# Kernel tuning notes

Hardware: AMD Instinct MI355X
Metric: run time of the kernel (lower is better)

Reference implementation:

```python
import jax, jax.numpy as jnp
import numpy as np

H = 16          # num heads
HD = 88         # head dim = 1408 / 16
IMG = 336
PATCH = 14
THETA = 10000.0
IDX = IMG // PATCH          # 24 patches per side
SEQ = IDX * IDX + 1         # 576 patches + 1 CLS slot = 577


def _vision_rope_cos_sin():
    # Faithful to HF Llama4VisionRotaryEmbedding (rope_type='llama4', complex64):
    # 2D rope over (x, y) patch coordinates; CLS token gets zero rotation.
    img_idx = np.arange(IDX * IDX, dtype=np.int64).reshape(-1, 1)
    img_idx = np.concatenate([img_idx, img_idx[:1]], axis=0)
    img_idx[-1, -1] = -2  # CLS token marker
    fx = img_idx % IDX
    fy = img_idx // IDX
    freq_dim = HD // 2  # 44
    rope_freq = 1.0 / (THETA ** (np.arange(0, freq_dim, 2)[: freq_dim // 2].astype(np.float64) / freq_dim))
    freqs_x = np.repeat((fx + 1)[..., None] * rope_freq[None, None, :], 2, axis=-1)
    freqs_y = np.repeat((fy + 1)[..., None] * rope_freq[None, None, :], 2, axis=-1)
    freqs = np.concatenate([freqs_x, freqs_y], axis=-1)[..., ::2]  # [SEQ, 1, HD//2]
    freqs = np.where(img_idx.reshape(-1, 1, 1) < 0, 0.0, freqs)
    return jnp.asarray(np.cos(freqs), jnp.float32), jnp.asarray(np.sin(freqs), jnp.float32)


def _apply_rope(x, cos, sin):
    # x: [B, S, H, HD]; treat last dim as HD//2 complex pairs, rotate by e^{i*freq}
    xr = x.reshape(*x.shape[:-1], HD // 2, 2)
    a, b = xr[..., 0], xr[..., 1]               # [B, S, H, HD//2]
    out_r = a * cos - b * sin                   # cos/sin [S,1,HD//2] broadcast over B,H
    out_i = a * sin + b * cos
    return jnp.stack([out_r, out_i], axis=-1).reshape(x.shape)


def setup_inputs() -> dict:
    key = jax.random.key(0)
    ks = jax.random.split(key, 9)
    D = H * HD  # 1408
    B, S = 32, SEQ
    s = 0.02
    return {
        "hidden_states": jax.random.normal(ks[0], (B, S, D), jnp.float32),
        "wq": jax.random.normal(ks[1], (D, D), jnp.float32) * s,
        "bq": jax.random.normal(ks[2], (D,), jnp.float32) * s,
        "wk": jax.random.normal(ks[3], (D, D), jnp.float32) * s,
        "bk": jax.random.normal(ks[4], (D,), jnp.float32) * s,
        "wv": jax.random.normal(ks[5], (D, D), jnp.float32) * s,
        "bv": jax.random.normal(ks[6], (D,), jnp.float32) * s,
        "wo": jax.random.normal(ks[7], (D, D), jnp.float32) * s,
        "bo": jax.random.normal(ks[8], (D,), jnp.float32) * s,
    }


def reference(hidden_states, wq, bq, wk, bk, wv, bv, wo, bo):
    B, S, D = hidden_states.shape
    cos, sin = _vision_rope_cos_sin()
    # QKV projections (torch Linear convention: y = x @ W.T + b)
    q = (hidden_states @ wq.T + bq).reshape(B, S, H, HD)
    k = (hidden_states @ wk.T + bk).reshape(B, S, H, HD)
    v = (hidden_states @ wv.T + bv).reshape(B, S, H, HD)
    q = _apply_rope(q, cos, sin)
    k = _apply_rope(k, cos, sin)
    # Full (non-causal) self-attention
    scores = jnp.einsum('bqhd,bkhd->bhqk', q, k) * (HD ** -0.5)
    probs = jax.nn.softmax(scores, axis=-1)
    attn = jnp.einsum('bhqk,bkhd->bqhd', probs, v).reshape(B, S, D)
    return attn @ wo.T + bo
```

## Files before the change

kernel.cpp:

```cpp
#include <hip/hip_runtime.h>
#include <hip/hip_bf16.h>
#include <cstdint>
#include <cstddef>

#define NHEADS 16
#define HDIM   88
#define SEQLEN 577
#define NBATCH 32
#define DMODEL 1408
#define MROWS  (NBATCH * SEQLEN)
#define MTILES 145
#define MPAD   (MTILES * 128)
#define SP     592
#define DP     96
#define NFREQ  44
#define NBH    (NBATCH * NHEADS)

typedef __attribute__((ext_vector_type(8))) short short8;
typedef __attribute__((ext_vector_type(4))) float floatx4;

__device__ __forceinline__ unsigned short f2bf(float f) {
    union { float f; unsigned u; } v; v.f = f;
    unsigned u = v.u;
    u += 0x7fffu + ((u >> 16) & 1u);
    return (unsigned short)(u >> 16);
}

__device__ __forceinline__ void gload_lds16(const void* g, void* lds) {
    __builtin_amdgcn_global_load_lds(
        (__attribute__((address_space(1))) unsigned int*)(void*)(g ? (void*)g : (void*)g),
        (__attribute__((address_space(3))) unsigned int*)lds, 16, 0, 0);
}

__global__ void l4v_rope_table(float* __restrict__ cos_t, float* __restrict__ sin_t) {
    int idx = blockIdx.x * blockDim.x + threadIdx.x;
    if (idx >= SEQLEN * NFREQ) return;
    int s = idx / NFREQ, j = idx % NFREQ;
    float ang = 0.0f;
    if (s != SEQLEN - 1) {
        int coord = (j < 22) ? (s % 24) : (s / 24);
        int i = (j < 22) ? j : j - 22;
        float rf = __expf(-(2.0f * (float)i / 44.0f) * 9.21034037197618f);
        ang = (float)(coord + 1) * rf;
    }
    cos_t[idx] = cosf(ang);
    sin_t[idx] = sinf(ang);
}

__global__ void l4v_cvt_bf16(const float* __restrict__ in, unsigned short* __restrict__ out, int n) {
    int i = (blockIdx.x * blockDim.x + threadIdx.x) * 4;
    if (i + 3 < n) {
        float4 f = *(const float4*)(in + i);
        ushort4 o;
        o.x = f2bf(f.x); o.y = f2bf(f.y); o.z = f2bf(f.z); o.w = f2bf(f.w);
        *(ushort4*)(out + i) = o;
    } else {
        for (; i < n; i++) out[i] = f2bf(in[i]);
    }
}

__global__ __launch_bounds__(256, 2)
void l4v_gemm128(const unsigned short* __restrict__ A,
                 const unsigned short* __restrict__ Bw,
                 const float* __restrict__ bias,
                 const float* __restrict__ cos_t,
                 const float* __restrict__ sin_t,
                 unsigned short* __restrict__ out_bf,
                 float* __restrict__ out_f32,
                 int mode)
{
    __shared__ __align__(16) unsigned short a_sm[128 * 32];
    __shared__ __align__(16) unsigned short b_sm[128 * 32];

    const int tid  = threadIdx.x;
    const int lane = tid & 63;
    const int w    = tid >> 6;
    const int quad = lane >> 4;
    const int c    = lane & 15;
    const int wr   = w >> 1;
    const int wc   = w & 1;
    const int m0   = blockIdx.y * 128;
    const int n0   = blockIdx.x * 128;

    floatx4 acc[4][4];
#pragma unroll
    for (int i = 0; i < 4; i++)
#pragma unroll
        for (int j = 0; j < 4; j++) acc[i][j] = (floatx4)0.0f;

    const int chunk0 = w * 128 + lane;
    const int chunk1 = w * 128 + 64 + lane;
    const int r0 = chunk0 >> 2, ch0 = chunk0 & 3;
    const int r1 = chunk1 >> 2, ch1 = chunk1 & 3;
    const unsigned short* Ab = A  + (size_t)m0 * DMODEL;
    const unsigned short* Bb = Bw + (size_t)n0 * DMODEL;

    for (int k0 = 0; k0 < DMODEL; k0 += 32) {
        gload_lds16(Ab + (size_t)r0 * DMODEL + k0 + ch0 * 8, a_sm + (w * 128) * 8);
        gload_lds16(Ab + (size_t)r1 * DMODEL + k0 + ch1 * 8, a_sm + (w * 128 + 64) * 8);
        gload_lds16(Bb + (size_t)r0 * DMODEL + k0 + ch0 * 8, b_sm + (w * 128) * 8);
        gload_lds16(Bb + (size_t)r1 * DMODEL + k0 + ch1 * 8, b_sm + (w * 128 + 64) * 8);
        __syncthreads();
        short8 af[4], bfr[4];
#pragma unroll
        for (int mt = 0; mt < 4; mt++)
            af[mt] = *(const short8*)(a_sm + (wr * 64 + mt * 16 + c) * 32 + quad * 8);
#pragma unroll
        for (int nt = 0; nt < 4; nt++)
            bfr[nt] = *(const short8*)(b_sm + (wc * 64 + nt * 16 + c) * 32 + quad * 8);
#pragma unroll
        for (int mt = 0; mt < 4; mt++)
#pragma unroll
            for (int nt = 0; nt < 4; nt++)
                acc[mt][nt] = __builtin_amdgcn_mfma_f32_16x16x32_bf16(af[mt], bfr[nt], acc[mt][nt], 0, 0, 0);
        __syncthreads();
    }

    if (mode == 3) {
#pragma unroll
        for (int mt = 0; mt < 4; mt++) {
            int mbase = m0 + wr * 64 + mt * 16 + quad * 4;
#pragma unroll
            for (int nt = 0; nt < 4; nt++) {
                int n = n0 + wc * 64 + nt * 16 + c;
                float bi = bias[n];
#pragma unroll
                for (int r = 0; r < 4; r++) {
                    int m = mbase + r;
                    if (m < MROWS) out_f32[(size_t)m * DMODEL + n] = acc[mt][nt][r] + bi;
                }
            }
        }
        return;
    }

    const bool rope = (mode < 2);
#pragma unroll
    for (int mt = 0; mt < 4; mt++) {
        int mbase = m0 + wr * 64 + mt * 16 + quad * 4;
#pragma unroll
        for (int nt = 0; nt < 4; nt++) {
            int n = n0 + wc * 64 + nt * 16 + c;
            float bi = bias[n];
            int h = n / HDIM, d = n % HDIM, j = d >> 1;
#pragma unroll
            for (int r = 0; r < 4; r++) {
                int m = mbase + r;
                int s = m % SEQLEN;
                int b = m / SEQLEN;
                float v = acc[mt][nt][r] + bi;
                float outv = v;
                if (rope) {
                    float pv = __shfl_xor(v, 1);
                    float cs = cos_t[s * NFREQ + j];
                    float sn = sin_t[s * NFREQ + j];
                    outv = ((d & 1) == 0) ? (v * cs - pv * sn) : (pv * sn + v * cs);
                }
                if (m < MROWS)
                    out_bf[((size_t)(b * NHEADS + h) * SP + s) * DP + d] = f2bf(outv);
            }
        }
    }
}

__global__ __launch_bounds__(256, 2)
void l4v_attn(const unsigned short* __restrict__ Q,
              const unsigned short* __restrict__ K,
              const unsigned short* __restrict__ V,
              unsigned short* __restrict__ Obuf)
{
    __shared__ __align__(16) unsigned short k_sm[64 * DP];
    __shared__ __align__(16) unsigned short v_sm[64 * DP];
    __shared__ __align__(16) unsigned short p_sm[4][16 * 64];

    const int tid  = threadIdx.x;
    const int lane = tid & 63;
    const int w    = tid >> 6;
    const int quad = lane >> 4;
    const int c    = lane & 15;
    const int qt   = blockIdx.x;
    const int bh   = blockIdx.y;
    const size_t base = (size_t)bh * SP * DP;

    short8 aq[3];
    {
        int qrow = qt * 64 + w * 16 + c;
        if (qrow > SP - 1) qrow = SP - 1;
#pragma unroll
        for (int ks = 0; ks < 3; ks++)
            aq[ks] = *(const short8*)(Q + base + (size_t)qrow * DP + ks * 32 + quad * 8);
    }

    float m_run[4], l_run[4];
    floatx4 o_acc[6];
#pragma unroll
    for (int r = 0; r < 4; r++) { m_run[r] = -INFINITY; l_run[r] = 0.0f; }
#pragma unroll
    for (int i = 0; i < 6; i++) o_acc[i] = (floatx4)0.0f;

    const float sl2e = 0.10660035817780522f * 1.4426950408889634f;

    for (int kt = 0; kt < 10; kt++) {
#pragma unroll
        for (int i = 0; i < 3; i++) {
            int chnk = w * 192 + i * 64 + lane;
            int row = chnk / 12, ch = chnk % 12;
            int krow = kt * 64 + row;
            if (krow > SP - 1) krow = SP - 1;
            gload_lds16(K + base + (size_t)krow * DP + ch * 8, k_sm + (w * 192 + i * 64) * 8);
            gload_lds16(V + base + (size_t)krow * DP + ch * 8, v_sm + (w * 192 + i * 64) * 8);
        }
        __syncthreads();

        floatx4 sc[4];
#pragma unroll
        for (int nt = 0; nt < 4; nt++) {
            sc[nt] = (floatx4)0.0f;
#pragma unroll
            for (int ks = 0; ks < 3; ks++) {
                short8 bk = *(const short8*)(k_sm + (nt * 16 + c) * DP + ks * 32 + quad * 8);
                sc[nt] = __builtin_amdgcn_mfma_f32_16x16x32_bf16(aq[ks], bk, sc[nt], 0, 0, 0);
            }
        }

        float t[4][4];
#pragma unroll
        for (int nt = 0; nt < 4; nt++) {
            int skcol = kt * 64 + nt * 16 + c;
            bool valid = (skcol < SEQLEN);
#pragma unroll
            for (int r = 0; r < 4; r++)
                t[nt][r] = valid ? sc[nt][r] * sl2e : -INFINITY;
        }

        float mnew[4], alpha[4];
#pragma unroll
        for (int r = 0; r < 4; r++) {
            float v = fmaxf(fmaxf(t[0][r], t[1][r]), fmaxf(t[2][r], t[3][r]));
#pragma unroll
            for (int off = 1; off < 16; off <<= 1) v = fmaxf(v, __shfl_xor(v, off));
            mnew[r] = fmaxf(m_run[r], v);
            alpha[r] = exp2f(m_run[r] - mnew[r]);
            m_run[r] = mnew[r];
        }

        float p[4][4];
#pragma unroll
        for (int nt = 0; nt < 4; nt++)
#pragma unroll
            for (int r = 0; r < 4; r++)
                p[nt][r] = exp2f(t[nt][r] - mnew[r]);

#pragma unroll
        for (int r = 0; r < 4; r++) {
            float sm = p[0][r] + p[1][r] + p[2][r] + p[3][r];
#pragma unroll
            for (int off = 1; off < 16; off <<= 1) sm += __shfl_xor(sm, off);
            l_run[r] = l_run[r] * alpha[r] + sm;
        }

#pragma unroll
        for (int nt = 0; nt < 4; nt++)
#pragma unroll
            for (int r = 0; r < 4; r++)
                p_sm[w][(quad * 4 + r) * 64 + nt * 16 + c] = f2bf(p[nt][r]);

#pragma unroll
        for (int i = 0; i < 6; i++)
#pragma unroll
            for (int r = 0; r < 4; r++)
                o_acc[i][r] *= alpha[r];

#pragma unroll
        for (int kp = 0; kp < 2; kp++) {
            short8 ap = *(const short8*)(&p_sm[w][c * 64 + kp * 32 + quad * 8]);
#pragma unroll
            for (int d2 = 0; d2 < 6; d2++) {
                short8 bv;
#pragma unroll
                for (int j = 0; j < 8; j++)
                    bv[j] = (short)v_sm[(kp * 32 + quad * 8 + j) * DP + d2 * 16 + c];
                o_acc[d2] = __builtin_amdgcn_mfma_f32_16x16x32_bf16(ap, bv, o_acc[d2], 0, 0, 0);
            }
        }
        __syncthreads();
    }

    const int b = bh >> 4, h = bh & 15;
#pragma unroll
    for (int r = 0; r < 4; r++) {
        int sq = qt * 64 + w * 16 + quad * 4 + r;
        float il = 1.0f / l_run[r];
        if (sq < SEQLEN) {
            size_t rowoff = ((size_t)b * SEQLEN + sq) * DMODEL + h * HDIM;
#pragma unroll
            for (int d2 = 0; d2 < 6; d2++) {
                int d = d2 * 16 + c;
                if (d < HDIM) Obuf[rowoff + d] = f2bf(o_acc[d2][r] * il);
            }
        }
    }
}

extern "C" void kernel_launch(void* const* d_in, const int* in_sizes, int n_in,
                              void* d_out, int out_size, void* d_ws, size_t ws_size,
                              hipStream_t stream)
{
    const float* hs = (const float*)d_in[0];
    const float* wq = (const float*)d_in[1];
    const float* bq = (const float*)d_in[2];
    const float* wk = (const float*)d_in[3];
    const float* bk = (const float*)d_in[4];
    const float* wv = (const float*)d_in[5];
    const float* bv = (const float*)d_in[6];
    const float* wo = (const float*)d_in[7];
    const float* bo = (const float*)d_in[8];
    float* out = (float*)d_out;

    char* ws = (char*)d_ws;
    size_t off = 0;
    auto alloc = [&](size_t bytes) -> char* {
        char* p = ws + off;
        off += (bytes + 255) & ~(size_t)255;
        return p;
    };

    unsigned short* hs_bf = (unsigned short*)alloc((size_t)MPAD * DMODEL * 2);
    unsigned short* wq_bf = (unsigned short*)alloc((size_t)DMODEL * DMODEL * 2);
    unsigned short* wk_bf = (unsigned short*)alloc((size_t)DMODEL * DMODEL * 2);
    unsigned short* wv_bf = (unsigned short*)alloc((size_t)DMODEL * DMODEL * 2);
    unsigned short* wo_bf = (unsigned short*)alloc((size_t)DMODEL * DMODEL * 2);
    unsigned short* qb    = (unsigned short*)alloc((size_t)NBH * SP * DP * 2);
    unsigned short* kb    = (unsigned short*)alloc((size_t)NBH * SP * DP * 2);
    unsigned short* vb    = (unsigned short*)alloc((size_t)NBH * SP * DP * 2);
    float* cos_t = (float*)alloc((size_t)SEQLEN * NFREQ * 4);
    float* sin_t = (float*)alloc((size_t)SEQLEN * NFREQ * 4);
    unsigned short* attn_bf = hs_bf;

    if (off > ws_size) return;

    l4v_rope_table<<<dim3((SEQLEN * NFREQ + 255) / 256), dim3(256), 0, stream>>>(cos_t, sin_t);

    const int nhs = MROWS * DMODEL;
    l4v_cvt_bf16<<<dim3(nhs / 4 / 256), dim3(256), 0, stream>>>(hs, hs_bf, nhs);
    const int nw = DMODEL * DMODEL;
    l4v_cvt_bf16<<<dim3(nw / 4 / 256), dim3(256), 0, stream>>>(wq, wq_bf, nw);
    l4v_cvt_bf16<<<dim3(nw / 4 / 256), dim3(256), 0, stream>>>(wk, wk_bf, nw);
    l4v_cvt_bf16<<<dim3(nw / 4 / 256), dim3(256), 0, stream>>>(wv, wv_bf, nw);
    l4v_cvt_bf16<<<dim3(nw / 4 / 256), dim3(256), 0, stream>>>(wo, wo_bf, nw);

    dim3 ggrid(DMODEL / 128, MTILES);
    l4v_gemm128<<<ggrid, dim3(256), 0, stream>>>(hs_bf, wq_bf, bq, cos_t, sin_t, qb, nullptr, 0);
    l4v_gemm128<<<ggrid, dim3(256), 0, stream>>>(hs_bf, wk_bf, bk, cos_t, sin_t, kb, nullptr, 1);
    l4v_gemm128<<<ggrid, dim3(256), 0, stream>>>(hs_bf, wv_bf, bv, cos_t, sin_t, vb, nullptr, 2);

    l4v_attn<<<dim3(10, NBH), dim3(256), 0, stream>>>(qb, kb, vb, attn_bf);

    l4v_gemm128<<<ggrid, dim3(256), 0, stream>>>(attn_bf, wo_bf, bo, cos_t, sin_t, nullptr, out, 3);
}
```

Before: 1.027 ms.

## Transpose V tile into swizzled LDS layout and zero-fill QKV padding

The attention kernel now transposes each 64-row V tile into a separate XOR-swizzled LDS buffer. The PV MFMA B-operand can then be read with two 4-element vector loads instead of eight strided scalar LDS reads, and the P scratch gets a padded row stride to reduce bank conflicts. The syncthreads moves from the end of the loop to before the PV stage. A new kernel zero-fills the padded rows and columns of the Q/K/V buffers so padding never holds garbage. This trades extra LDS capacity and an extra write pass per tile for cheaper PV operand fetches, and it may affect occupancy.

```diff
diff --git a/kernel.cpp b/kernel.cpp
--- a/kernel.cpp
+++ b/kernel.cpp
@@ -15,8 +15,10 @@
 #define DP     96
 #define NFREQ  44
 #define NBH    (NBATCH * NHEADS)
+#define PADELEMS 6056
 
 typedef __attribute__((ext_vector_type(8))) short short8;
+typedef __attribute__((ext_vector_type(4))) short short4v;
 typedef __attribute__((ext_vector_type(4))) float floatx4;
 
 __device__ __forceinline__ unsigned short f2bf(float f) {
@@ -57,6 +59,24 @@
     } else {
         for (; i < n; i++) out[i] = f2bf(in[i]);
     }
+}
+
+__global__ void l4v_padzero(unsigned short* __restrict__ qb,
+                            unsigned short* __restrict__ kb,
+                            unsigned short* __restrict__ vb) {
+    int idx = blockIdx.x * blockDim.x + threadIdx.x;
+    if (idx >= NBH * PADELEMS) return;
+    int bh = idx / PADELEMS, r = idx % PADELEMS;
+    size_t off;
+    if (r < 15 * 96) {
+        int row = SEQLEN + r / 96, col = r % 96;
+        off = ((size_t)bh * SP + row) * DP + col;
+    } else {
+        int rr = r - 15 * 96;
+        int row = rr / 8, col = 88 + (rr % 8);
+        off = ((size_t)bh * SP + row) * DP + col;
+    }
+    qb[off] = 0; kb[off] = 0; vb[off] = 0;
 }
 
 __global__ __launch_bounds__(256, 2)
@@ -171,7 +191,8 @@
 {
     __shared__ __align__(16) unsigned short k_sm[64 * DP];
     __shared__ __align__(16) unsigned short v_sm[64 * DP];
-    __shared__ __align__(16) unsigned short p_sm[4][16 * 64];
+    __shared__ __align__(16) unsigned short v_tr[96 * 68];
+    __shared__ __align__(16) unsigned short p_sm[4][16 * 68];
 
     const int tid  = threadIdx.x;
     const int lane = tid & 63;
@@ -223,6 +244,19 @@
             }
         }
 
+#pragma unroll
+        for (int i = 0; i < 3; i++) {
+            int chnk = w * 192 + i * 64 + lane;
+            int srow = chnk / 12, ch = chnk % 12;
+            short8 vv = *(const short8*)(v_sm + srow * DP + ch * 8);
+#pragma unroll
+            for (int jj = 0; jj < 8; jj++) {
+                int d = ch * 8 + jj;
+                v_tr[d * 68 + (((srow >> 2) ^ (d & 15)) << 2) + (srow & 3)] =
+                    (unsigned short)vv[jj];
+            }
+        }
+
         float t[4][4];
 #pragma unroll
         for (int nt = 0; nt < 4; nt++) {
@@ -263,7 +297,7 @@
         for (int nt = 0; nt < 4; nt++)
 #pragma unroll
             for (int r = 0; r < 4; r++)
-                p_sm[w][(quad * 4 + r) * 64 + nt * 16 + c] = f2bf(p[nt][r]);
+                p_sm[w][(quad * 4 + r) * 68 + nt * 16 + c] = f2bf(p[nt][r]);
 
 #pragma unroll
         for (int i = 0; i < 6; i++)
@@ -271,19 +305,29 @@
             for (int r = 0; r < 4; r++)
                 o_acc[i][r] *= alpha[r];
 
+        __syncthreads();
+
 #pragma unroll
         for (int kp = 0; kp < 2; kp++) {
-            short8 ap = *(const short8*)(&p_sm[w][c * 64 + kp * 32 + quad * 8]);
+            short8 ap;
+            {
+                short4v lo = *(const short4v*)(&p_sm[w][c * 68 + kp * 32 + quad * 8]);
+                short4v hi = *(const short4v*)(&p_sm[w][c * 68 + kp * 32 + quad * 8 + 4]);
+#pragma unroll
+                for (int t4 = 0; t4 < 4; t4++) { ap[t4] = lo[t4]; ap[t4 + 4] = hi[t4]; }
+            }
 #pragma unroll
             for (int d2 = 0; d2 < 6; d2++) {
+                int drow = d2 * 16 + c;
+                int c4 = kp * 8 + quad * 2;
+                short4v lo = *(const short4v*)(v_tr + drow * 68 + (((c4 + 0) ^ c) << 2));
+                short4v hi = *(const short4v*)(v_tr + drow * 68 + (((c4 + 1) ^ c) << 2));
                 short8 bv;
 #pragma unroll
-                for (int j = 0; j < 8; j++)
-                    bv[j] = (short)v_sm[(kp * 32 + quad * 8 + j) * DP + d2 * 16 + c];
+                for (int t4 = 0; t4 < 4; t4++) { bv[t4] = lo[t4]; bv[t4 + 4] = hi[t4]; }
                 o_acc[d2] = __builtin_amdgcn_mfma_f32_16x16x32_bf16(ap, bv, o_acc[d2], 0, 0, 0);
             }
         }
-        __syncthreads();
     }
 
     const int b = bh >> 4, h = bh & 15;
@@ -332,7 +376,7 @@
     unsigned short* wo_bf = (unsigned short*)alloc((size_t)DMODEL * DMODEL * 2);
     unsigned short* qb    = (unsigned short*)alloc((size_t)NBH * SP * DP * 2);
     unsigned short* kb    = (unsigned short*)alloc((size_t)NBH * SP * DP * 2);
-    unsigned short* vb    = (unsigned short*)alloc((size_t)NBH * SP * DP * 2);
+    unsigned short* vbuf  = (unsigned short*)alloc((size_t)NBH * SP * DP * 2);
     float* cos_t = (float*)alloc((size_t)SEQLEN * NFREQ * 4);
     float* sin_t = (float*)alloc((size_t)SEQLEN * NFREQ * 4);
     unsigned short* attn_bf = hs_bf;
@@ -340,6 +384,7 @@
     if (off > ws_size) return;
 
     l4v_rope_table<<<dim3((SEQLEN * NFREQ + 255) / 256), dim3(256), 0, stream>>>(cos_t, sin_t);
+    l4v_padzero<<<dim3((NBH * PADELEMS + 255) / 256), dim3(256), 0, stream>>>(qb, kb, vbuf);
 
     const int nhs = MROWS * DMODEL;
     l4v_cvt_bf16<<<dim3(nhs / 4 / 256), dim3(256), 0, stream>>>(hs, hs_bf, nhs);
@@ -352,9 +397,9 @@
     dim3 ggrid(DMODEL / 128, MTILES);
     l4v_gemm128<<<ggrid, dim3(256), 0, stream>>>(hs_bf, wq_bf, bq, cos_t, sin_t, qb, nullptr, 0);
     l4v_gemm128<<<ggrid, dim3(256), 0, stream>>>(hs_bf, wk_bf, bk, cos_t, sin_t, kb, nullptr, 1);
-    l4v_gemm128<<<ggrid, dim3(256), 0, stream>>>(hs_bf, wv_bf, bv, cos_t, sin_t, vb, nullptr, 2);
-
-    l4v_attn<<<dim3(10, NBH), dim3(256), 0, stream>>>(qb, kb, vb, attn_bf);
+    l4v_gemm128<<<ggrid, dim3(256), 0, stream>>>(hs_bf, wv_bf, bv, cos_t, sin_t, vbuf, nullptr, 2);
+
+    l4v_attn<<<dim3(10, NBH), dim3(256), 0, stream>>>(qb, kb, vbuf, attn_bf);
 
     l4v_gemm128<<<ggrid, dim3(256), 0, stream>>>(attn_bf, wo_bf, bo, cos_t, sin_t, nullptr, out, 3);
 }
```

Result: slower. 1.207 ms (+17.5%).
